# Optimization experiments

Hardware: AMD Instinct MI355X
Metric: run time of the kernel (lower is better)

## Reference

```python
import jax, jax.numpy as jnp
import numpy as np

LRU_DIM = 256
HIDDEN = 256
H = 64
N = LRU_DIM // H  # 4 (even, per assert)
R_MIN, R_MAX, MAX_PHASE = 0.9, 0.999, 6.28
BSZ, T = 8, 4096


def _rotate_half(x):
    # interleaved pairs: [x0,x1,x2,x3,...] -> [-x1,x0,-x3,x2,...]
    r = jnp.stack([-x[..., 1::2], x[..., 0::2]], axis=-1)
    return r.reshape(x.shape)


def _mix_sequence(gamma, thetas, Us):
    # gamma: scalar, thetas: (N/2,), Us: (T,B,N) -> (T,B,N)
    Tlen = Us.shape[0]
    gammas = jnp.broadcast_to(gamma, (Tlen,))
    ths = jnp.broadcast_to(thetas, (Tlen,) + thetas.shape)

    def binf(a, b):
        gi, ti, xi = a
        gj, tj, xj = b
        theta = jnp.repeat(tj, 2, axis=-1)            # (T, N): [t0,t0,t1,t1,...]
        sin = jnp.sin(theta)[..., None, :]            # (T,1,N)
        cos = jnp.cos(theta)[..., None, :]
        acc = gj[..., None, None] * (cos * xi + sin * _rotate_half(xi)) + xj
        return (gi * gj, ti + tj, acc)

    _, _, res = jax.lax.associative_scan(binf, (gammas, ths, Us), axis=0)
    return res


def setup_inputs() -> dict:
    key = jax.random.key(0)
    ks = jax.random.split(key, 7)
    scale = 1.0 / np.sqrt(HIDDEN + LRU_DIM)
    u = jax.random.normal(ks[0], (BSZ, HIDDEN, T), dtype=jnp.float32)
    thetas_log = jnp.log(jax.random.uniform(ks[1], (H, N // 2), minval=0.01, maxval=1.0) * MAX_PHASE).astype(jnp.float32)
    P_param = (jax.random.normal(ks[2], (H, N, N), dtype=jnp.float32) / np.sqrt(LRU_DIM + N)).astype(jnp.float32)
    B_param = (jax.random.normal(ks[3], (H, N, HIDDEN), dtype=jnp.float32) * scale).astype(jnp.float32)
    C = (jax.random.normal(ks[4], (HIDDEN, LRU_DIM), dtype=jnp.float32) * scale).astype(jnp.float32)
    D = jax.random.normal(ks[5], (HIDDEN,), dtype=jnp.float32)
    u1 = jax.random.uniform(ks[6], (H,))
    gamma_log = (np.log(-np.log(R_MAX)) + u1 * (np.log(-np.log(R_MIN)) - np.log(-np.log(R_MAX)))).astype(jnp.float32)
    return {"u": u, "thetas_log": thetas_log, "P_param": P_param,
            "B_param": B_param, "C": C, "D": D, "gamma_log": gamma_log}


def reference(u, thetas_log, P_param, B_param, C, D, gamma_log):
    Bsz, hidden, Tlen = u.shape
    ut = jnp.transpose(u, (0, 2, 1))                       # (B,T,Dh)
    gamma = jnp.exp(-jnp.exp(gamma_log))                   # (H,)
    trace_per_head = jnp.sum(B_param * B_param, axis=(1, 2))  # tr(B B^T) per head
    norm = jnp.sqrt((1.0 - gamma ** 2) / trace_per_head)
    B_norm = norm[:, None, None] * B_param                 # (H,N,Dh)
    skew = P_param - jnp.swapaxes(P_param, 1, 2)
    P = jax.vmap(jax.scipy.linalg.expm)(skew)              # (H,N,N), orthogonal
    Us = jnp.einsum('HnD,BTD->HTBn', B_norm, ut)           # (H,T,B,N)
    Us = jnp.einsum('HNn,HTBn->HTBN', P, Us)               # == einsum with P^T as in torch
    thetas = jnp.exp(thetas_log)                           # (H,N/2)
    y = jax.vmap(_mix_sequence)(gamma, thetas, Us)         # (H,T,B,N)
    y = jnp.einsum('HNn,HTBN->HTBn', P, y)
    y = jnp.transpose(y, (2, 1, 0, 3)).reshape(Bsz, Tlen, -1)  # (B,T,lru_dim)
    y = jnp.einsum('Dn,BTn->BTD', C, y) + D * ut
    return jnp.transpose(y, (0, 2, 1))                     # (B,Dh,T)
```

## Files before the change

### kernel.cpp

```cpp
#include <hip/hip_runtime.h>
#include <hip/hip_bf16.h>
#include <math.h>


typedef __attribute__((ext_vector_type(8))) short short8;
typedef __attribute__((ext_vector_type(4))) float f32x4;

#define TLEN 4096
#define LCH 64
#define NCH 64
#define BSZ 8
#define LDK 264
#define LDW 132

constexpr int MB_OFF   = 0;
constexpr int CB_OFF   = 32768;
constexpr int AP_OFF   = 65536;
constexpr int ALP_OFF  = AP_OFF + 65 * 256;
constexpr int TOT_OFF  = ALP_OFF + 65 * 256;
constexpr int PL_OFF   = TOT_OFF + NCH * BSZ * 256;
constexpr int NORM_OFF = PL_OFF + 1024;
constexpr int S_OFF    = NORM_OFF + 64;

__device__ __forceinline__ float bfbits2f(unsigned int bits16) {
  union { unsigned int u; float f; } v; v.u = bits16 << 16; return v.f;
}
__device__ __forceinline__ unsigned int f2bfbits(float f) {
  union { float f; unsigned int u; } v; v.f = f;
  return (v.u + 0x7fffu + ((v.u >> 16) & 1u)) >> 16;
}
__device__ __forceinline__ unsigned int pack2(float x, float y) {
  return f2bfbits(x) | (f2bfbits(y) << 16);
}

__global__ __launch_bounds__(256) void k0a_precompute(
    const float* __restrict__ thetas_log, const float* __restrict__ P_param,
    const float* __restrict__ B_param, const float* __restrict__ gamma_log,
    float* __restrict__ ws) {
  __shared__ float tracep[64][4];
  __shared__ double gamma_d[64];
  const int tid = threadIdx.x;
  {
    int h = tid >> 2, q = tid & 3;
    const float* bp = B_param + (h * 4 + q) * 256;
    float s = 0.f;
    for (int i = 0; i < 256; ++i) { float v = bp[i]; s += v * v; }
    tracep[h][q] = s;
  }
  __syncthreads();
  if (tid < 64) {
    int h = tid;
    double g = exp(-exp((double)gamma_log[h]));
    gamma_d[h] = g;
    double tr = (double)tracep[h][0] + tracep[h][1] + tracep[h][2] + tracep[h][3];
    ws[NORM_OFF + h] = (float)sqrt((1.0 - g * g) / tr);
    double A[4][4], E[4][4], Tm[4][4];
    for (int i = 0; i < 4; ++i)
      for (int j = 0; j < 4; ++j)
        A[i][j] = (double)P_param[h * 16 + i * 4 + j] - (double)P_param[h * 16 + j * 4 + i];
    double fro = 0.0;
    for (int i = 0; i < 4; ++i) for (int j = 0; j < 4; ++j) fro += A[i][j] * A[i][j];
    fro = sqrt(fro);
    int s = 0;
    while (fro > 0.25 && s < 30) { fro *= 0.5; ++s; }
    double scl = 1.0;
    for (int q2 = 0; q2 < s; ++q2) scl *= 0.5;
    for (int i = 0; i < 4; ++i) for (int j = 0; j < 4; ++j) A[i][j] *= scl;
    for (int i = 0; i < 4; ++i)
      for (int j = 0; j < 4; ++j) { E[i][j] = (i == j) ? 1.0 : 0.0; Tm[i][j] = E[i][j]; }
    for (int k = 1; k <= 16; ++k) {
      double Tn[4][4];
      for (int i = 0; i < 4; ++i)
        for (int j = 0; j < 4; ++j) {
          double acc = 0.0;
          for (int m = 0; m < 4; ++m) acc += Tm[i][m] * A[m][j];
          Tn[i][j] = acc / (double)k;
        }
      for (int i = 0; i < 4; ++i)
        for (int j = 0; j < 4; ++j) { Tm[i][j] = Tn[i][j]; E[i][j] += Tn[i][j]; }
    }
    for (int q2 = 0; q2 < s; ++q2) {
      double E2[4][4];
      for (int i = 0; i < 4; ++i)
        for (int j = 0; j < 4; ++j) {
          double acc = 0.0;
          for (int m = 0; m < 4; ++m) acc += E[i][m] * E[m][j];
          E2[i][j] = acc;
        }
      for (int i = 0; i < 4; ++i) for (int j = 0; j < 4; ++j) E[i][j] = E2[i][j];
    }
    for (int i = 0; i < 4; ++i)
      for (int j = 0; j < 4; ++j) ws[PL_OFF + h * 16 + i * 4 + j] = (float)E[i][j];
  }
  __syncthreads();
  if (tid < 128) {
    int h = tid >> 1, p = tid & 1;
    double th = exp((double)thetas_log[h * 2 + p]);
    double g = gamma_d[h];
    double ar = g * cos(th), ai = g * sin(th);
    float2* Apw = (float2*)(ws + AP_OFF);
    float2* ALp = (float2*)(ws + ALP_OFF);
    double xr = 1.0, xi = 0.0;
    Apw[tid] = make_float2(1.f, 0.f);
    for (int j = 1; j <= LCH; ++j) {
      double nr = xr * ar - xi * ai, ni = xr * ai + xi * ar;
      xr = nr; xi = ni;
      Apw[j * 128 + tid] = make_float2((float)xr, (float)xi);
    }
    double br = xr, bi = xi;
    xr = 1.0; xi = 0.0;
    ALp[tid] = make_float2(1.f, 0.f);
    for (int k = 1; k <= NCH; ++k) {
      double nr = xr * br - xi * bi, ni = xr * bi + xi * br;
      xr = nr; xi = ni;
      ALp[k * 128 + tid] = make_float2((float)xr, (float)xi);
    }
  }
}

__global__ __launch_bounds__(256) void k0b_mats(
    const float* __restrict__ B_param, const float* __restrict__ C,
    float* __restrict__ ws) {
  const float* Pl  = ws + PL_OFF;
  const float* nrm = ws + NORM_OFF;
  unsigned short* Mbf = (unsigned short*)(ws + MB_OFF);
  unsigned short* Cbf = (unsigned short*)(ws + CB_OFF);
  const int blk = blockIdx.x, tid = threadIdx.x;
  if (blk < 16) {
    for (int rr = 0; rr < 16; ++rr) {
      int r = blk * 16 + rr, h = r >> 2, N = r & 3;
      float acc = 0.f;
      for (int n = 0; n < 4; ++n)
        acc += Pl[h * 16 + N * 4 + n] * B_param[(h * 4 + n) * 256 + tid];
      Mbf[r * 256 + tid] = (unsigned short)f2bfbits(nrm[h] * acc);
    }
  } else {
    int h = tid >> 2;
    int N = tid & 3;
    for (int rr = 0; rr < 16; ++rr) {
      int Do = (blk - 16) * 16 + rr;
      float acc = 0.f;
      for (int n = 0; n < 4; ++n)
        acc += C[Do * 256 + (tid & ~3) + n] * Pl[h * 16 + N * 4 + n];
      Cbf[Do * 256 + tid] = (unsigned short)f2bfbits(acc);
    }
  }
}

__global__ __launch_bounds__(256) void k1_mfma(
    const float* __restrict__ u, float* __restrict__ ws) {
  __shared__ __align__(16) unsigned char smem[64 * LDK * 2];
  unsigned short* us = (unsigned short*)smem;
  unsigned int*   wd = (unsigned int*)smem;

  const int c = blockIdx.x, b = blockIdx.y;
  const int t0 = c * LCH;
  const int tid = threadIdx.x;
  const int L = tid & 63;
  const int w = __builtin_amdgcn_readfirstlane(tid >> 6);
  const int qh = L >> 4, l15 = L & 15;

  {
    const int kbase = tid >> 4;
    const int t4 = (tid & 15) * 4;
#pragma unroll
    for (int i = 0; i < 16; ++i) {
      int d = kbase + i * 16;
      float4 v = *(const float4*)(u + (size_t)(b * 256 + d) * TLEN + t0 + t4);
      float vv[4] = {v.x, v.y, v.z, v.w};
#pragma unroll
      for (int dt = 0; dt < 4; ++dt) {
        int t = t4 + dt;
        us[t * LDK + (d ^ ((t & 3) << 3))] = (unsigned short)f2bfbits(vv[dt]);
      }
    }
  }
  __syncthreads();

  f32x4 acc[4][4];
#pragma unroll
  for (int rt = 0; rt < 4; ++rt)
#pragma unroll
    for (int tt = 0; tt < 4; ++tt) acc[rt][tt] = (f32x4){0.f, 0.f, 0.f, 0.f};
  {
    const unsigned short* Mbf = (const unsigned short*)(ws + MB_OFF);
#pragma unroll
    for (int ks = 0; ks < 8; ++ks) {
      short8 af[4], bf[4];
#pragma unroll
      for (int rt = 0; rt < 4; ++rt)
        af[rt] = *(const short8*)(Mbf + (size_t)(w * 64 + rt * 16 + l15) * 256 + ks * 32 + qh * 8);
#pragma unroll
      for (int tt = 0; tt < 4; ++tt) {
        int row = tt * 16 + l15;
        int col = (ks * 32 + qh * 8) ^ ((row & 3) << 3);
        bf[tt] = *(const short8*)(us + row * LDK + col);
      }
#pragma unroll
      for (int rt = 0; rt < 4; ++rt)
#pragma unroll
        for (int tt = 0; tt < 4; ++tt)
          acc[rt][tt] = __builtin_amdgcn_mfma_f32_16x16x32_bf16(af[rt], bf[tt], acc[rt][tt], 0, 0, 0);
    }
  }
  __syncthreads();

#pragma unroll
  for (int rt = 0; rt < 4; ++rt) {
    int pbase = w * 32 + rt * 8 + qh * 2;
#pragma unroll
    for (int tt = 0; tt < 4; ++tt) {
      int t = tt * 16 + l15;
      f32x4 a4 = acc[rt][tt];
      wd[t * LDW + pbase]     = pack2(a4[0], a4[1]);
      wd[t * LDW + pbase + 1] = pack2(a4[2], a4[3]);
    }
  }
  __syncthreads();

  if (tid < 128) {
    const int p = tid;
    const float2* Apw = (const float2*)(ws + AP_OFF);
    float2 a = Apw[128 + p];
    float zr = 0.f, zi = 0.f;
#pragma unroll
    for (int t = 0; t < LCH; ++t) {
      unsigned int wv = wd[t * LDW + p];
      float wr = bfbits2f(wv & 0xffffu), wi = bfbits2f(wv >> 16);
      float nr = fmaf(a.x, zr, fmaf(-a.y, zi, wr));
      float ni = fmaf(a.x, zi, fmaf(a.y, zr, wi));
      zr = nr; zi = ni;
      wd[t * LDW + p] = pack2(zr, zi);
    }
    ((float2*)(ws + TOT_OFF))[(c * BSZ + b) * 128 + p] = make_float2(zr, zi);
  }
  __syncthreads();

  unsigned int* Sg = (unsigned int*)(ws + S_OFF);
#pragma unroll
  for (int i = 0; i < 32; ++i) {
    int idx = tid + 256 * i;
    int t = idx >> 7, q = idx & 127;
    Sg[(size_t)(t0 + t) * 1024 + b * 128 + q] = wd[t * LDW + q];
  }
}

__global__ __launch_bounds__(256) void k3_mfma(
    const float* __restrict__ u, const float* __restrict__ Dv,
    const float* __restrict__ ws, float* __restrict__ out) {
  __shared__ __align__(16) unsigned char smem[64 * LDK * 2];
  unsigned int* zd = (unsigned int*)smem;

  const int c = blockIdx.x, b = blockIdx.y;
  const int t0 = c * LCH;
  const int tid = threadIdx.x;
  const int L = tid & 63;
  const int w = __builtin_amdgcn_readfirstlane(tid >> 6);
  const int qh = L >> 4, l15 = L & 15;
  const unsigned int* Sg = (const unsigned int*)(ws + S_OFF);

  if (tid < 128) {
    const int p = tid;
    float cr = 0.f, ci = 0.f;
    const float2* ALp = (const float2*)(ws + ALP_OFF);
    const float2* Tot = (const float2*)(ws + TOT_OFF);
    for (int cp = 0; cp < c; ++cp) {
      float2 al = ALp[(c - 1 - cp) * 128 + p];
      float2 tv = Tot[(cp * BSZ + b) * 128 + p];
      cr = fmaf(al.x, tv.x, fmaf(-al.y, tv.y, cr));
      ci = fmaf(al.x, tv.y, fmaf(al.y, tv.x, ci));
    }
    const float2* Apw = (const float2*)(ws + AP_OFF);
#pragma unroll
    for (int t = 0; t < LCH; ++t) {
      unsigned int wv = Sg[(size_t)(t0 + t) * 1024 + b * 128 + p];
      float2 ap = Apw[(t + 1) * 128 + p];
      float sr = fmaf(ap.x, cr, fmaf(-ap.y, ci, bfbits2f(wv & 0xffffu)));
      float si = fmaf(ap.x, ci, fmaf(ap.y, cr, bfbits2f(wv >> 16)));
      zd[t * LDW + p] = pack2(sr, si);
    }
  }
  __syncthreads();

  f32x4 acc[4][4];
#pragma unroll
  for (int rt = 0; rt < 4; ++rt)
#pragma unroll
    for (int tt = 0; tt < 4; ++tt) acc[rt][tt] = (f32x4){0.f, 0.f, 0.f, 0.f};
  {
    const unsigned short* Cbf = (const unsigned short*)(ws + CB_OFF);
    const unsigned short* zs  = (const unsigned short*)smem;
#pragma unroll
    for (int ks = 0; ks < 8; ++ks) {
      short8 af[4], bf[4];
#pragma unroll
      for (int rt = 0; rt < 4; ++rt)
        af[rt] = *(const short8*)(Cbf + (size_t)(w * 64 + rt * 16 + l15) * 256 + ks * 32 + qh * 8);
#pragma unroll
      for (int tt = 0; tt < 4; ++tt)
        bf[tt] = *(const short8*)(zs + (tt * 16 + l15) * LDK + ks * 32 + qh * 8);
#pragma unroll
      for (int rt = 0; rt < 4; ++rt)
#pragma unroll
        for (int tt = 0; tt < 4; ++tt)
          acc[rt][tt] = __builtin_amdgcn_mfma_f32_16x16x32_bf16(af[rt], bf[tt], acc[rt][tt], 0, 0, 0);
    }
  }

  float dv[4][4];
#pragma unroll
  for (int rt = 0; rt < 4; ++rt)
#pragma unroll
    for (int q = 0; q < 4; ++q) dv[rt][q] = Dv[w * 64 + rt * 16 + qh * 4 + q];
#pragma unroll
  for (int rt = 0; rt < 4; ++rt) {
    int Dbase = w * 64 + rt * 16 + qh * 4;
#pragma unroll
    for (int tt = 0; tt < 4; ++tt) {
      int t = tt * 16 + l15;
      f32x4 a4 = acc[rt][tt];
      size_t obase = (size_t)(b * 256 + Dbase) * TLEN + t0 + t;
#pragma unroll
      for (int q = 0; q < 4; ++q)
        out[obase + (size_t)q * TLEN] = a4[q] + dv[rt][q] * u[obase + (size_t)q * TLEN];
    }
  }
}

extern "C" void kernel_launch(void* const* d_in, const int* in_sizes, int n_in,
                              void* d_out, int out_size, void* d_ws, size_t ws_size,
                              hipStream_t stream) {
  const float* u          = (const float*)d_in[0];
  const float* thetas_log = (const float*)d_in[1];
  const float* P_param    = (const float*)d_in[2];
  const float* B_param    = (const float*)d_in[3];
  const float* C          = (const float*)d_in[4];
  const float* Dvec       = (const float*)d_in[5];
  const float* gamma_log  = (const float*)d_in[6];
  float* out = (float*)d_out;
  float* ws  = (float*)d_ws;

  hipLaunchKernelGGL(k0a_precompute, dim3(1), dim3(256), 0, stream,
                     thetas_log, P_param, B_param, gamma_log, ws);
  hipLaunchKernelGGL(k0b_mats, dim3(32), dim3(256), 0, stream, B_param, C, ws);
  hipLaunchKernelGGL(k1_mfma, dim3(NCH, BSZ), dim3(256), 0, stream, u, ws);
  hipLaunchKernelGGL(k3_mfma, dim3(NCH, BSZ), dim3(256), 0, stream, u, Dvec, ws, out);
}
```

Measured before the change: 170.9 us.

## Recompute chunk scan in output kernel instead of storing intermediate states

The output kernel now recomputes the first projection GEMM and the in-chunk scan from u, so the large per-timestep state buffer no longer has to be written to and read back from global memory. Chunk length is halved and the chunk count doubled to give more blocks, and an occupancy hint is added. The two setup kernels are merged into one per-head kernel that uses warp-shuffle reductions. The trade-off is that the first GEMM runs twice and u is read an extra time. The carry loop over previous chunks also gets longer with more chunks.

```diff
diff --git a/kernel.cpp b/kernel.cpp
--- a/kernel.cpp
+++ b/kernel.cpp
@@ -1,5 +1,4 @@
 #include <hip/hip_runtime.h>
-#include <hip/hip_bf16.h>
 #include <math.h>
 
 
@@ -7,8 +6,8 @@
 typedef __attribute__((ext_vector_type(4))) float f32x4;
 
 #define TLEN 4096
-#define LCH 64
-#define NCH 64
+#define LCH 32
+#define NCH 128
 #define BSZ 8
 #define LDK 264
 #define LDW 132
@@ -16,11 +15,8 @@
 constexpr int MB_OFF   = 0;
 constexpr int CB_OFF   = 32768;
 constexpr int AP_OFF   = 65536;
-constexpr int ALP_OFF  = AP_OFF + 65 * 256;
-constexpr int TOT_OFF  = ALP_OFF + 65 * 256;
-constexpr int PL_OFF   = TOT_OFF + NCH * BSZ * 256;
-constexpr int NORM_OFF = PL_OFF + 1024;
-constexpr int S_OFF    = NORM_OFF + 64;
+constexpr int ALP_OFF  = AP_OFF + (LCH + 1) * 256;
+constexpr int TOT_OFF  = ALP_OFF + (NCH + 1) * 256;
 
 __device__ __forceinline__ float bfbits2f(unsigned int bits16) {
   union { unsigned int u; float f; } v; v.u = bits16 << 16; return v.f;
@@ -33,27 +29,26 @@
   return f2bfbits(x) | (f2bfbits(y) << 16);
 }
 
-__global__ __launch_bounds__(256) void k0a_precompute(
+__global__ __launch_bounds__(256) void k0_setup(
     const float* __restrict__ thetas_log, const float* __restrict__ P_param,
-    const float* __restrict__ B_param, const float* __restrict__ gamma_log,
-    float* __restrict__ ws) {
-  __shared__ float tracep[64][4];
-  __shared__ double gamma_d[64];
+    const float* __restrict__ B_param, const float* __restrict__ C,
+    const float* __restrict__ gamma_log, float* __restrict__ ws) {
+  const int h = blockIdx.x;
   const int tid = threadIdx.x;
-  {
-    int h = tid >> 2, q = tid & 3;
-    const float* bp = B_param + (h * 4 + q) * 256;
-    float s = 0.f;
-    for (int i = 0; i < 256; ++i) { float v = bp[i]; s += v * v; }
-    tracep[h][q] = s;
-  }
-  __syncthreads();
-  if (tid < 64) {
-    int h = tid;
-    double g = exp(-exp((double)gamma_log[h]));
-    gamma_d[h] = g;
-    double tr = (double)tracep[h][0] + tracep[h][1] + tracep[h][2] + tracep[h][3];
-    ws[NORM_OFF + h] = (float)sqrt((1.0 - g * g) / tr);
+  __shared__ float red[4];
+  __shared__ float Psh[16];
+  __shared__ float nrmsh;
+
+  {
+    float4 v = *(const float4*)(B_param + (size_t)h * 1024 + tid * 4);
+    float s = v.x * v.x + v.y * v.y + v.z * v.z + v.w * v.w;
+#pragma unroll
+    for (int off = 32; off > 0; off >>= 1) s += __shfl_down(s, off);
+    if ((tid & 63) == 0) red[tid >> 6] = s;
+  }
+  __syncthreads();
+
+  if (tid == 0) {
     double A[4][4], E[4][4], Tm[4][4];
     for (int i = 0; i < 4; ++i)
       for (int j = 0; j < 4; ++j)
@@ -90,82 +85,80 @@
       for (int i = 0; i < 4; ++i) for (int j = 0; j < 4; ++j) E[i][j] = E2[i][j];
     }
     for (int i = 0; i < 4; ++i)
-      for (int j = 0; j < 4; ++j) ws[PL_OFF + h * 16 + i * 4 + j] = (float)E[i][j];
-  }
-  __syncthreads();
-  if (tid < 128) {
-    int h = tid >> 1, p = tid & 1;
-    double th = exp((double)thetas_log[h * 2 + p]);
-    double g = gamma_d[h];
+      for (int j = 0; j < 4; ++j) Psh[i * 4 + j] = (float)E[i][j];
+  } else if (tid == 64 || tid == 65) {
+    const int p = h * 2 + (tid - 64);
+    double th = exp((double)thetas_log[p]);
+    double g = exp(-exp((double)gamma_log[h]));
     double ar = g * cos(th), ai = g * sin(th);
     float2* Apw = (float2*)(ws + AP_OFF);
     float2* ALp = (float2*)(ws + ALP_OFF);
     double xr = 1.0, xi = 0.0;
-    Apw[tid] = make_float2(1.f, 0.f);
+    Apw[p] = make_float2(1.f, 0.f);
     for (int j = 1; j <= LCH; ++j) {
       double nr = xr * ar - xi * ai, ni = xr * ai + xi * ar;
       xr = nr; xi = ni;
-      Apw[j * 128 + tid] = make_float2((float)xr, (float)xi);
+      Apw[j * 128 + p] = make_float2((float)xr, (float)xi);
     }
     double br = xr, bi = xi;
     xr = 1.0; xi = 0.0;
-    ALp[tid] = make_float2(1.f, 0.f);
+    ALp[p] = make_float2(1.f, 0.f);
     for (int k = 1; k <= NCH; ++k) {
       double nr = xr * br - xi * bi, ni = xr * bi + xi * br;
       xr = nr; xi = ni;
-      ALp[k * 128 + tid] = make_float2((float)xr, (float)xi);
-    }
-  }
-}
-
-__global__ __launch_bounds__(256) void k0b_mats(
-    const float* __restrict__ B_param, const float* __restrict__ C,
-    float* __restrict__ ws) {
-  const float* Pl  = ws + PL_OFF;
-  const float* nrm = ws + NORM_OFF;
+      ALp[k * 128 + p] = make_float2((float)xr, (float)xi);
+    }
+  } else if (tid == 128) {
+    double g = exp(-exp((double)gamma_log[h]));
+    double tr = (double)red[0] + red[1] + red[2] + red[3];
+    nrmsh = (float)sqrt((1.0 - g * g) / tr);
+  }
+  __syncthreads();
+
   unsigned short* Mbf = (unsigned short*)(ws + MB_OFF);
-  unsigned short* Cbf = (unsigned short*)(ws + CB_OFF);
-  const int blk = blockIdx.x, tid = threadIdx.x;
-  if (blk < 16) {
-    for (int rr = 0; rr < 16; ++rr) {
-      int r = blk * 16 + rr, h = r >> 2, N = r & 3;
-      float acc = 0.f;
-      for (int n = 0; n < 4; ++n)
-        acc += Pl[h * 16 + N * 4 + n] * B_param[(h * 4 + n) * 256 + tid];
-      Mbf[r * 256 + tid] = (unsigned short)f2bfbits(nrm[h] * acc);
-    }
-  } else {
-    int h = tid >> 2;
-    int N = tid & 3;
-    for (int rr = 0; rr < 16; ++rr) {
-      int Do = (blk - 16) * 16 + rr;
-      float acc = 0.f;
-      for (int n = 0; n < 4; ++n)
-        acc += C[Do * 256 + (tid & ~3) + n] * Pl[h * 16 + N * 4 + n];
-      Cbf[Do * 256 + tid] = (unsigned short)f2bfbits(acc);
-    }
-  }
-}
-
-__global__ __launch_bounds__(256) void k1_mfma(
-    const float* __restrict__ u, float* __restrict__ ws) {
-  __shared__ __align__(16) unsigned char smem[64 * LDK * 2];
+  unsigned int*   Cbd = (unsigned int*)(ws + CB_OFF);
+  {
+    float b0 = B_param[(h * 4 + 0) * 256 + tid];
+    float b1 = B_param[(h * 4 + 1) * 256 + tid];
+    float b2 = B_param[(h * 4 + 2) * 256 + tid];
+    float b3 = B_param[(h * 4 + 3) * 256 + tid];
+    float nrm = nrmsh;
+#pragma unroll
+    for (int N = 0; N < 4; ++N) {
+      float acc = Psh[N * 4 + 0] * b0 + Psh[N * 4 + 1] * b1 +
+                  Psh[N * 4 + 2] * b2 + Psh[N * 4 + 3] * b3;
+      Mbf[(h * 4 + N) * 256 + tid] = (unsigned short)f2bfbits(nrm * acc);
+    }
+  }
+  {
+    float4 cv = *(const float4*)(C + (size_t)tid * 256 + h * 4);
+    float o[4];
+#pragma unroll
+    for (int N = 0; N < 4; ++N)
+      o[N] = cv.x * Psh[N * 4 + 0] + cv.y * Psh[N * 4 + 1] +
+             cv.z * Psh[N * 4 + 2] + cv.w * Psh[N * 4 + 3];
+    Cbd[(tid * 256 + h * 4) >> 1]       = pack2(o[0], o[1]);
+    Cbd[((tid * 256 + h * 4) >> 1) + 1] = pack2(o[2], o[3]);
+  }
+}
+
+__device__ __forceinline__ void stage_gemm1_scan(
+    const float* __restrict__ u, const float* __restrict__ ws,
+    unsigned char* smem, int c, int b, int tid,
+    float* zr_out, float* zi_out) {
   unsigned short* us = (unsigned short*)smem;
   unsigned int*   wd = (unsigned int*)smem;
-
-  const int c = blockIdx.x, b = blockIdx.y;
   const int t0 = c * LCH;
-  const int tid = threadIdx.x;
   const int L = tid & 63;
   const int w = __builtin_amdgcn_readfirstlane(tid >> 6);
   const int qh = L >> 4, l15 = L & 15;
 
   {
-    const int kbase = tid >> 4;
-    const int t4 = (tid & 15) * 4;
-#pragma unroll
-    for (int i = 0; i < 16; ++i) {
-      int d = kbase + i * 16;
+    const int dg = tid >> 3;
+    const int t4 = (tid & 7) * 4;
+#pragma unroll
+    for (int i = 0; i < 8; ++i) {
+      int d = dg + i * 32;
       float4 v = *(const float4*)(u + (size_t)(b * 256 + d) * TLEN + t0 + t4);
       float vv[4] = {v.x, v.y, v.z, v.w};
 #pragma unroll
@@ -177,21 +170,21 @@
   }
   __syncthreads();
 
-  f32x4 acc[4][4];
+  f32x4 acc[4][2];
 #pragma unroll
   for (int rt = 0; rt < 4; ++rt)
 #pragma unroll
-    for (int tt = 0; tt < 4; ++tt) acc[rt][tt] = (f32x4){0.f, 0.f, 0.f, 0.f};
+    for (int tt = 0; tt < 2; ++tt) acc[rt][tt] = (f32x4){0.f, 0.f, 0.f, 0.f};
   {
     const unsigned short* Mbf = (const unsigned short*)(ws + MB_OFF);
 #pragma unroll
     for (int ks = 0; ks < 8; ++ks) {
-      short8 af[4], bf[4];
+      short8 af[4], bf[2];
 #pragma unroll
       for (int rt = 0; rt < 4; ++rt)
         af[rt] = *(const short8*)(Mbf + (size_t)(w * 64 + rt * 16 + l15) * 256 + ks * 32 + qh * 8);
 #pragma unroll
-      for (int tt = 0; tt < 4; ++tt) {
+      for (int tt = 0; tt < 2; ++tt) {
         int row = tt * 16 + l15;
         int col = (ks * 32 + qh * 8) ^ ((row & 3) << 3);
         bf[tt] = *(const short8*)(us + row * LDK + col);
@@ -199,7 +192,7 @@
 #pragma unroll
       for (int rt = 0; rt < 4; ++rt)
 #pragma unroll
-        for (int tt = 0; tt < 4; ++tt)
+        for (int tt = 0; tt < 2; ++tt)
           acc[rt][tt] = __builtin_amdgcn_mfma_f32_16x16x32_bf16(af[rt], bf[tt], acc[rt][tt], 0, 0, 0);
     }
   }
@@ -209,7 +202,7 @@
   for (int rt = 0; rt < 4; ++rt) {
     int pbase = w * 32 + rt * 8 + qh * 2;
 #pragma unroll
-    for (int tt = 0; tt < 4; ++tt) {
+    for (int tt = 0; tt < 2; ++tt) {
       int t = tt * 16 + l15;
       f32x4 a4 = acc[rt][tt];
       wd[t * LDW + pbase]     = pack2(a4[0], a4[1]);
@@ -218,11 +211,11 @@
   }
   __syncthreads();
 
+  float zr = 0.f, zi = 0.f;
   if (tid < 128) {
     const int p = tid;
     const float2* Apw = (const float2*)(ws + AP_OFF);
     float2 a = Apw[128 + p];
-    float zr = 0.f, zi = 0.f;
 #pragma unroll
     for (int t = 0; t < LCH; ++t) {
       unsigned int wv = wd[t * LDW + p];
@@ -232,24 +225,26 @@
       zr = nr; zi = ni;
       wd[t * LDW + p] = pack2(zr, zi);
     }
-    ((float2*)(ws + TOT_OFF))[(c * BSZ + b) * 128 + p] = make_float2(zr, zi);
-  }
-  __syncthreads();
-
-  unsigned int* Sg = (unsigned int*)(ws + S_OFF);
-#pragma unroll
-  for (int i = 0; i < 32; ++i) {
-    int idx = tid + 256 * i;
-    int t = idx >> 7, q = idx & 127;
-    Sg[(size_t)(t0 + t) * 1024 + b * 128 + q] = wd[t * LDW + q];
-  }
-}
-
-__global__ __launch_bounds__(256) void k3_mfma(
+  }
+  *zr_out = zr; *zi_out = zi;
+}
+
+__global__ __launch_bounds__(256, 4) void k1_mfma(
+    const float* __restrict__ u, float* __restrict__ ws) {
+  __shared__ __align__(16) unsigned char smem[LCH * LDK * 2];
+  const int c = blockIdx.x, b = blockIdx.y;
+  const int tid = threadIdx.x;
+  float zr, zi;
+  stage_gemm1_scan(u, ws, smem, c, b, tid, &zr, &zi);
+  if (tid < 128)
+    ((float2*)(ws + TOT_OFF))[(c * BSZ + b) * 128 + tid] = make_float2(zr, zi);
+}
+
+__global__ __launch_bounds__(256, 4) void k3_mfma(
     const float* __restrict__ u, const float* __restrict__ Dv,
     const float* __restrict__ ws, float* __restrict__ out) {
-  __shared__ __align__(16) unsigned char smem[64 * LDK * 2];
-  unsigned int* zd = (unsigned int*)smem;
+  __shared__ __align__(16) unsigned char smem[LCH * LDK * 2];
+  unsigned int* wd = (unsigned int*)smem;
 
   const int c = blockIdx.x, b = blockIdx.y;
   const int t0 = c * LCH;
@@ -257,10 +252,14 @@
   const int L = tid & 63;
   const int w = __builtin_amdgcn_readfirstlane(tid >> 6);
   const int qh = L >> 4, l15 = L & 15;
-  const unsigned int* Sg = (const unsigned int*)(ws + S_OFF);
-
-  if (tid < 128) {
-    const int p = tid;
+
+  float zr_dummy, zi_dummy;
+  stage_gemm1_scan(u, ws, smem, c, b, tid, &zr_dummy, &zi_dummy);
+  __syncthreads();
+
+  {
+    const int p = tid & 127;
+    const int thalf = (tid >> 7) * 16;
     float cr = 0.f, ci = 0.f;
     const float2* ALp = (const float2*)(ws + ALP_OFF);
     const float2* Tot = (const float2*)(ws + TOT_OFF);
@@ -272,37 +271,38 @@
     }
     const float2* Apw = (const float2*)(ws + AP_OFF);
 #pragma unroll
-    for (int t = 0; t < LCH; ++t) {
-      unsigned int wv = Sg[(size_t)(t0 + t) * 1024 + b * 128 + p];
+    for (int tt2 = 0; tt2 < 16; ++tt2) {
+      int t = thalf + tt2;
+      unsigned int wv = wd[t * LDW + p];
       float2 ap = Apw[(t + 1) * 128 + p];
       float sr = fmaf(ap.x, cr, fmaf(-ap.y, ci, bfbits2f(wv & 0xffffu)));
       float si = fmaf(ap.x, ci, fmaf(ap.y, cr, bfbits2f(wv >> 16)));
-      zd[t * LDW + p] = pack2(sr, si);
-    }
-  }
-  __syncthreads();
-
-  f32x4 acc[4][4];
+      wd[t * LDW + p] = pack2(sr, si);
+    }
+  }
+  __syncthreads();
+
+  f32x4 acc[4][2];
 #pragma unroll
   for (int rt = 0; rt < 4; ++rt)
 #pragma unroll
-    for (int tt = 0; tt < 4; ++tt) acc[rt][tt] = (f32x4){0.f, 0.f, 0.f, 0.f};
+    for (int tt = 0; tt < 2; ++tt) acc[rt][tt] = (f32x4){0.f, 0.f, 0.f, 0.f};
   {
     const unsigned short* Cbf = (const unsigned short*)(ws + CB_OFF);
     const unsigned short* zs  = (const unsigned short*)smem;
 #pragma unroll
     for (int ks = 0; ks < 8; ++ks) {
-      short8 af[4], bf[4];
+      short8 af[4], bf[2];
 #pragma unroll
       for (int rt = 0; rt < 4; ++rt)
         af[rt] = *(const short8*)(Cbf + (size_t)(w * 64 + rt * 16 + l15) * 256 + ks * 32 + qh * 8);
 #pragma unroll
-      for (int tt = 0; tt < 4; ++tt)
+      for (int tt = 0; tt < 2; ++tt)
         bf[tt] = *(const short8*)(zs + (tt * 16 + l15) * LDK + ks * 32 + qh * 8);
 #pragma unroll
       for (int rt = 0; rt < 4; ++rt)
 #pragma unroll
-        for (int tt = 0; tt < 4; ++tt)
+        for (int tt = 0; tt < 2; ++tt)
           acc[rt][tt] = __builtin_amdgcn_mfma_f32_16x16x32_bf16(af[rt], bf[tt], acc[rt][tt], 0, 0, 0);
     }
   }
@@ -316,7 +316,7 @@
   for (int rt = 0; rt < 4; ++rt) {
     int Dbase = w * 64 + rt * 16 + qh * 4;
 #pragma unroll
-    for (int tt = 0; tt < 4; ++tt) {
+    for (int tt = 0; tt < 2; ++tt) {
       int t = tt * 16 + l15;
       f32x4 a4 = acc[rt][tt];
       size_t obase = (size_t)(b * 256 + Dbase) * TLEN + t0 + t;
@@ -340,9 +340,8 @@
   float* out = (float*)d_out;
   float* ws  = (float*)d_ws;
 
-  hipLaunchKernelGGL(k0a_precompute, dim3(1), dim3(256), 0, stream,
-                     thetas_log, P_param, B_param, gamma_log, ws);
-  hipLaunchKernelGGL(k0b_mats, dim3(32), dim3(256), 0, stream, B_param, C, ws);
+  hipLaunchKernelGGL(k0_setup, dim3(64), dim3(256), 0, stream,
+                     thetas_log, P_param, B_param, C, gamma_log, ws);
   hipLaunchKernelGGL(k1_mfma, dim3(NCH, BSZ), dim3(256), 0, stream, u, ws);
   hipLaunchKernelGGL(k3_mfma, dim3(NCH, BSZ), dim3(256), 0, stream, u, Dvec, ws, out);
 }
```

After: 196.6 us. 15.0% more time.
